# Performance work log

Hardware: AMD Instinct MI355X
Metric: run time of the kernel (lower is better)

## Reference

```python
import jax, jax.numpy as jnp
import numpy as np

D_K = 64  # key dim -> temperature = sqrt(64) = 8.0


def setup_inputs() -> dict:
    key = jax.random.key(0)
    k1, k2, k3, k4 = jax.random.split(key, 4)
    N, P, d_k, d_v = 4, 4096, 64, 256
    k_src = jax.random.normal(k1, (N, P, d_k), dtype=jnp.float32)
    v_src = jax.random.normal(k2, (N, P, d_v), dtype=jnp.float32)
    q_tgr = jax.random.normal(k3, (N, P, d_k), dtype=jnp.float32)
    # 1x1 conv (d_v -> d_v) == per-position linear; kaiming-style init
    W_fc = jax.random.normal(k4, (d_v, d_v), dtype=jnp.float32) * (1.0 / np.sqrt(d_v))
    b_fc = jnp.zeros((d_v,), dtype=jnp.float32)
    return {"k_src": k_src, "v_src": v_src, "q_tgr": q_tgr, "W_fc": W_fc, "b_fc": b_fc}


def reference(k_src, v_src, q_tgr, W_fc, b_fc):
    temperature = jnp.asarray(np.sqrt(D_K), dtype=q_tgr.dtype)
    # scaled dot-product attention: [N,P,P] scores (mask=None, dropout=eval/identity)
    attn = jnp.einsum("npd,nqd->npq", q_tgr, k_src) / temperature
    attn = jax.nn.softmax(attn, axis=2)
    out = jnp.einsum("npq,nqc->npc", attn, v_src)  # [N,P,d_v]
    # fc: 1x1 conv over (N*P, C, 1, 1) == linear over channel dim
    out = jnp.einsum("npc,oc->npo", out, W_fc) + b_fc
    return out
```

## Files before the change

kernel.cpp:

```cpp
#include <hip/hip_runtime.h>
#include <hip/hip_bf16.h>

#define NB 4
#define PSEQ 4096
#define DK 64
#define DV 256

typedef __attribute__((ext_vector_type(8))) short short8;
typedef __attribute__((ext_vector_type(16))) float f32x16;
typedef __attribute__((ext_vector_type(4))) unsigned int uint4v;

__device__ __forceinline__ float bf2f(unsigned short u) {
    union { unsigned int i; float f; } v; v.i = ((unsigned int)u) << 16; return v.f;
}
__device__ __forceinline__ unsigned short f2bf(float f) {
    union { float f; unsigned int i; } v; v.f = f;
    return (unsigned short)((v.i + 0x7fffu + ((v.i >> 16) & 1u)) >> 16);
}

__device__ __forceinline__ short8 gload16(const void* p) {
    short8 r;
    asm volatile("global_load_dwordx4 %0, %1, off"
                 : "=v"(r) : "v"(p) : "memory");
    return r;
}

__global__ __launch_bounds__(256) void prep_all(
    const float* __restrict__ q, const float* __restrict__ k,
    const float* __restrict__ wfc, const float* __restrict__ v,
    unsigned short* __restrict__ Qh, unsigned short* __restrict__ Ql,
    unsigned short* __restrict__ Kp,
    unsigned short* __restrict__ Wb, unsigned short* __restrict__ Vp) {
    __shared__ float tile[64][65];
    const int b = blockIdx.x, tid = threadIdx.x;
    if (b < 1024) {
        const int i = (b * 256 + tid) * 4;
        float4 x = *reinterpret_cast<const float4*>(q + i);
        ushort4 h, l;
        h.x = f2bf(x.x); l.x = f2bf(x.x - bf2f(h.x));
        h.y = f2bf(x.y); l.y = f2bf(x.y - bf2f(h.y));
        h.z = f2bf(x.z); l.z = f2bf(x.z - bf2f(h.z));
        h.w = f2bf(x.w); l.w = f2bf(x.w - bf2f(h.w));
        *reinterpret_cast<ushort4*>(Qh + i) = h;
        *reinterpret_cast<ushort4*>(Ql + i) = l;
    } else if (b < 1536) {
        const int idx = b - 1024;
        const int n = idx >> 7, g = idx & 127;
        const int d = tid >> 6, lane = tid & 63;
        const int l31 = lane & 31, hi = lane >> 5;
        const float* src = k + ((size_t)(n * PSEQ + g * 32 + l31)) * DK + d * 16 + hi * 8;
        float x[8];
        *reinterpret_cast<float4*>(&x[0]) = *reinterpret_cast<const float4*>(src);
        *reinterpret_cast<float4*>(&x[4]) = *reinterpret_cast<const float4*>(src + 4);
        short8 o;
#pragma unroll
        for (int j = 0; j < 8; ++j) o[j] = (short)f2bf(x[j]);
        *reinterpret_cast<short8*>(
            Kp + (((size_t)n * 512 + g * 4 + d) * 64 + lane) * 8) = o;
    } else if (b < 1600) {
        const int i = ((b - 1536) * 256 + tid) * 4;
        float4 x = *reinterpret_cast<const float4*>(wfc + i);
        ushort4 h;
        h.x = f2bf(x.x); h.y = f2bf(x.y); h.z = f2bf(x.z); h.w = f2bf(x.w);
        *reinterpret_cast<ushort4*>(Wb + i) = h;
    } else {
        const int vtid = b - 1600;
        const int k0 = (vtid & 63) * 64, c0 = ((vtid >> 6) & 3) * 64, n = vtid >> 8;
        const int gb = (vtid & 63) * 2;
        const int cb = ((vtid >> 6) & 3) * 2;
        const float* vn = v + (size_t)n * PSEQ * DV;
        const int tx = tid & 15, ty = tid >> 4;
#pragma unroll
        for (int rep = 0; rep < 4; ++rep) {
            int r = ty + rep * 16;
            float4 d = *reinterpret_cast<const float4*>(vn + (size_t)(k0 + r) * DV + c0 + tx * 4);
            tile[r][tx * 4 + 0] = d.x; tile[r][tx * 4 + 1] = d.y;
            tile[r][tx * 4 + 2] = d.z; tile[r][tx * 4 + 3] = d.w;
        }
        __syncthreads();
#pragma unroll
        for (int uu = 0; uu < 2; ++uu) {
            const int u = tid * 2 + uu;
            const int lane = u & 63;
            const int slot = (u >> 6) & 1;
            const int c32l = (u >> 7) & 1;
            const int gl   = (u >> 8) & 1;
            const int l31 = lane & 31, hi = lane >> 5;
            const int keyl = gl * 32 + slot * 16 + hi * 8;
            const int chl = c32l * 32 + l31;
            short8 o;
#pragma unroll
            for (int j = 0; j < 8; ++j) o[j] = (short)f2bf(tile[keyl + j][chl]);
            *reinterpret_cast<short8*>(
                Vp + ((((size_t)n * 128 + gb + gl) * 8 + cb + c32l) * 2 + slot) * 512
                   + lane * 8) = o;
        }
    }
}

__global__ __launch_bounds__(256, 2) void attn_wave(
    const unsigned short* __restrict__ Kp,
    const unsigned short* __restrict__ Qh,
    const unsigned short* __restrict__ Ql,
    const unsigned short* __restrict__ Vp,
    const unsigned short* __restrict__ Wg,
    const float* __restrict__ Bg,
    float* __restrict__ Og)
{
    __shared__ float Of32[32][256];
    __shared__ unsigned short Omrg[32][260];
    __shared__ float Lsh[32];

    const int tid = threadIdx.x;
    const int w = tid >> 6;
    const int lane = tid & 63;
    const int l31 = lane & 31;
    const int hi = lane >> 5;
    const int kh = w >> 1;
    const int ch = w & 1;

    const int id = blockIdx.x;
    const int n = (id & 7) >> 1;
    const int q0 = ((id >> 3) * 2 + (id & 1)) * 32;

    if (tid < 32) Lsh[tid] = 0.f;
    __syncthreads();

    const unsigned short* Kpn = Kp + (size_t)n * 512 * 512;
    const unsigned short* Vpn = Vp + (size_t)n * 128 * 8 * 2 * 512;

    short8 qhf[4], qlf[4];
#pragma unroll
    for (int d = 0; d < 4; ++d) {
        const size_t a = ((size_t)n * PSEQ + q0 + l31) * DK + d * 16 + hi * 8;
        qhf[d] = *reinterpret_cast<const short8*>(Qh + a);
        qlf[d] = *reinterpret_cast<const short8*>(Ql + a);
    }

    const f32x16 Z16 = {0.f,0.f,0.f,0.f, 0.f,0.f,0.f,0.f,
                        0.f,0.f,0.f,0.f, 0.f,0.f,0.f,0.f};
    f32x16 oacc[4];
#pragma unroll
    for (int ct = 0; ct < 4; ++ct) oacc[ct] = Z16;

    float lsum = 0.f;
    const float SC = 0.125f * 1.44269504088896340736f;

    auto issueK = [&](int kt, short8 (&kf)[4]) {
        const int g = kh * 64 + kt;
#pragma unroll
        for (int d = 0; d < 4; ++d)
            kf[d] = gload16(Kpn + ((size_t)(g * 4 + d) * 64 + lane) * 8);
    };

    auto TILE = [&](int kt, short8 (&kfC)[4], short8 (&kfN)[4]) {
        asm volatile("s_waitcnt vmcnt(0)" ::: "memory");
        __builtin_amdgcn_sched_barrier(0);

        const int g = kh * 64 + kt;

        short8 vv[8];
#pragma unroll
        for (int ct = 0; ct < 4; ++ct) {
            const size_t vb = (((size_t)g * 8 + ch * 4 + ct) * 2) * 512;
            vv[ct]     = gload16(Vpn + vb + lane * 8);
            vv[4 + ct] = gload16(Vpn + vb + 512 + lane * 8);
        }

        f32x16 s = Z16;
        __builtin_amdgcn_s_setprio(1);
#pragma unroll
        for (int d = 0; d < 4; ++d)
            s = __builtin_amdgcn_mfma_f32_32x32x16_bf16(kfC[d], qhf[d], s, 0, 0, 0);
#pragma unroll
        for (int d = 0; d < 4; ++d)
            s = __builtin_amdgcn_mfma_f32_32x32x16_bf16(kfC[d], qlf[d], s, 0, 0, 0);
        __builtin_amdgcn_s_setprio(0);

        issueK(kt < 63 ? kt + 1 : 63, kfN);

        unsigned int pk[8];
        float lacc = 0.f;
#pragma unroll
        for (int j = 0; j < 8; ++j) {
            float p0 = exp2f(s[2 * j] * SC);
            float p1 = exp2f(s[2 * j + 1] * SC);
            lacc += p0 + p1;
            asm("v_cvt_pk_bf16_f32 %0, %1, %2" : "=v"(pk[j]) : "v"(p0), "v"(p1));
        }
        lsum += lacc;
        asm volatile("v_permlane32_swap_b32 %0, %1" : "+v"(pk[0]), "+v"(pk[2]));
        asm volatile("v_permlane32_swap_b32 %0, %1" : "+v"(pk[1]), "+v"(pk[3]));
        asm volatile("v_permlane32_swap_b32 %0, %1" : "+v"(pk[4]), "+v"(pk[6]));
        asm volatile("v_permlane32_swap_b32 %0, %1" : "+v"(pk[5]), "+v"(pk[7]));
        union { uint4v u; short8 s8; } cvt0, cvt1;
        cvt0.u = (uint4v){pk[0], pk[1], pk[2], pk[3]};
        cvt1.u = (uint4v){pk[4], pk[5], pk[6], pk[7]};
        const short8 pa0 = cvt0.s8, pa1 = cvt1.s8;

        asm volatile("s_waitcnt vmcnt(4)" ::: "memory");
        __builtin_amdgcn_sched_barrier(0);

        __builtin_amdgcn_s_setprio(1);
#pragma unroll
        for (int ct = 0; ct < 4; ++ct)
            oacc[ct] = __builtin_amdgcn_mfma_f32_32x32x16_bf16(pa0, vv[ct], oacc[ct], 0, 0, 0);
#pragma unroll
        for (int ct = 0; ct < 4; ++ct)
            oacc[ct] = __builtin_amdgcn_mfma_f32_32x32x16_bf16(pa1, vv[4 + ct], oacc[ct], 0, 0, 0);
        __builtin_amdgcn_s_setprio(0);
    };

    short8 kfA[4], kfB[4];
    issueK(0, kfA);

#pragma unroll 1
    for (int kt = 0; kt < 64; kt += 2) {
        TILE(kt, kfA, kfB);
        TILE(kt + 1, kfB, kfA);
    }
    asm volatile("s_waitcnt vmcnt(0)" ::: "memory");

    lsum += __shfl_xor(lsum, 32, 64);
    if (ch == 0 && lane < 32) atomicAdd(&Lsh[l31], lsum);

    const int cb0 = ch * 128;
    if (kh == 0) {
#pragma unroll
        for (int ct = 0; ct < 4; ++ct)
#pragma unroll
            for (int r = 0; r < 16; ++r) {
                const int row = (r & 3) + 8 * (r >> 2) + 4 * hi;
                Of32[row][cb0 + ct * 32 + l31] = oacc[ct][r];
            }
    }
    __syncthreads();
    if (kh == 1) {
#pragma unroll
        for (int ct = 0; ct < 4; ++ct)
#pragma unroll
            for (int r = 0; r < 16; ++r) {
                const int row = (r & 3) + 8 * (r >> 2) + 4 * hi;
                Of32[row][cb0 + ct * 32 + l31] += oacc[ct][r];
            }
    }
    __syncthreads();

    {
        const int row = tid >> 3;
        const int col0 = (tid & 7) * 32;
        const float il = 1.0f / Lsh[row];
#pragma unroll
        for (int j = 0; j < 8; ++j) {
            float4 xv = *reinterpret_cast<const float4*>(&Of32[row][col0 + j * 4]);
            ushort4 o;
            o.x = f2bf(xv.x * il); o.y = f2bf(xv.y * il);
            o.z = f2bf(xv.z * il); o.w = f2bf(xv.w * il);
            *reinterpret_cast<ushort4*>(&Omrg[row][col0 + j * 4]) = o;
        }
    }
    __syncthreads();

    f32x16 fa0 = Z16, fa1 = Z16;
#pragma unroll
    for (int slot = 0; slot < 16; ++slot) {
        short8 af = *reinterpret_cast<const short8*>(&Omrg[l31][slot * 16 + hi * 8]);
        short8 w0 = *reinterpret_cast<const short8*>(
            Wg + (size_t)(w * 64 + l31) * DV + slot * 16 + hi * 8);
        short8 w1 = *reinterpret_cast<const short8*>(
            Wg + (size_t)(w * 64 + 32 + l31) * DV + slot * 16 + hi * 8);
        fa0 = __builtin_amdgcn_mfma_f32_32x32x16_bf16(af, w0, fa0, 0, 0, 0);
        fa1 = __builtin_amdgcn_mfma_f32_32x32x16_bf16(af, w1, fa1, 0, 0, 0);
    }
    {
        const float b0 = Bg[w * 64 + l31], b1 = Bg[w * 64 + 32 + l31];
#pragma unroll
        for (int r = 0; r < 16; ++r) {
            const int row = (r & 3) + 8 * (r >> 2) + 4 * hi;
            const size_t orow = ((size_t)n * PSEQ + q0 + row) * DV;
            Og[orow + w * 64 + l31]      = fa0[r] + b0;
            Og[orow + w * 64 + 32 + l31] = fa1[r] + b1;
        }
    }
}

extern "C" void kernel_launch(void* const* d_in, const int* in_sizes, int n_in,
                              void* d_out, int out_size, void* d_ws, size_t ws_size,
                              hipStream_t stream) {
    const float* k_src = (const float*)d_in[0];
    const float* v_src = (const float*)d_in[1];
    const float* q_tgr = (const float*)d_in[2];
    const float* W_fc  = (const float*)d_in[3];
    const float* b_fc  = (const float*)d_in[4];
    float* out = (float*)d_out;

    char* wsb = (char*)d_ws;
    unsigned short* Vp = (unsigned short*)(wsb);
    unsigned short* Qh = (unsigned short*)(wsb + 8388608);
    unsigned short* Ql = (unsigned short*)(wsb + 10485760);
    unsigned short* Kp = (unsigned short*)(wsb + 12582912);
    unsigned short* Wb = (unsigned short*)(wsb + 14680064);

    prep_all<<<2624, 256, 0, stream>>>(q_tgr, k_src, W_fc, v_src,
                                       Qh, Ql, Kp, Wb, Vp);
    attn_wave<<<512, 256, 0, stream>>>(Kp, Qh, Ql, Vp, Wb, b_fc, out);
}
```

Baseline: 180.0 us.

## Split attention blocks by value-channel half and combine FC output with atomics

Each block now owns one 32-row query tile and one half of the value channels. Its four waves split the key range into quarters instead of a 2x2 key/channel split, which doubles the grid to 1024 blocks. Partial FC products over the two channel halves are accumulated into the output with float atomics, so a memset of the output is added before the launch. The aim is more parallelism and occupancy, but the QK scores and softmax are now computed twice per query tile, and the change adds a four-step serialized LDS reduction plus atomic-add traffic.

```diff
diff --git a/kernel.cpp b/kernel.cpp
--- a/kernel.cpp
+++ b/kernel.cpp
@@ -107,8 +107,8 @@
     const float* __restrict__ Bg,
     float* __restrict__ Og)
 {
-    __shared__ float Of32[32][256];
-    __shared__ unsigned short Omrg[32][260];
+    __shared__ float Of32[32][128];
+    __shared__ unsigned short Omrg[32][132];
     __shared__ float Lsh[32];
 
     const int tid = threadIdx.x;
@@ -116,12 +116,11 @@
     const int lane = tid & 63;
     const int l31 = lane & 31;
     const int hi = lane >> 5;
-    const int kh = w >> 1;
-    const int ch = w & 1;
 
     const int id = blockIdx.x;
-    const int n = (id & 7) >> 1;
-    const int q0 = ((id >> 3) * 2 + (id & 1)) * 32;
+    const int n   = (id & 7) >> 1;
+    const int chb = id & 1;
+    const int q0  = (id >> 3) * 32;
 
     if (tid < 32) Lsh[tid] = 0.f;
     __syncthreads();
@@ -147,7 +146,7 @@
     const float SC = 0.125f * 1.44269504088896340736f;
 
     auto issueK = [&](int kt, short8 (&kf)[4]) {
-        const int g = kh * 64 + kt;
+        const int g = w * 32 + kt;
 #pragma unroll
         for (int d = 0; d < 4; ++d)
             kf[d] = gload16(Kpn + ((size_t)(g * 4 + d) * 64 + lane) * 8);
@@ -157,12 +156,12 @@
         asm volatile("s_waitcnt vmcnt(0)" ::: "memory");
         __builtin_amdgcn_sched_barrier(0);
 
-        const int g = kh * 64 + kt;
+        const int g = w * 32 + kt;
 
         short8 vv[8];
 #pragma unroll
         for (int ct = 0; ct < 4; ++ct) {
-            const size_t vb = (((size_t)g * 8 + ch * 4 + ct) * 2) * 512;
+            const size_t vb = (((size_t)g * 8 + chb * 4 + ct) * 2) * 512;
             vv[ct]     = gload16(Vpn + vb + lane * 8);
             vv[4 + ct] = gload16(Vpn + vb + 512 + lane * 8);
         }
@@ -177,7 +176,7 @@
             s = __builtin_amdgcn_mfma_f32_32x32x16_bf16(kfC[d], qlf[d], s, 0, 0, 0);
         __builtin_amdgcn_s_setprio(0);
 
-        issueK(kt < 63 ? kt + 1 : 63, kfN);
+        issueK(kt < 31 ? kt + 1 : 31, kfN);
 
         unsigned int pk[8];
         float lacc = 0.f;
@@ -215,43 +214,62 @@
     issueK(0, kfA);
 
 #pragma unroll 1
-    for (int kt = 0; kt < 64; kt += 2) {
+    for (int kt = 0; kt < 32; kt += 2) {
         TILE(kt, kfA, kfB);
         TILE(kt + 1, kfB, kfA);
     }
     asm volatile("s_waitcnt vmcnt(0)" ::: "memory");
 
     lsum += __shfl_xor(lsum, 32, 64);
-    if (ch == 0 && lane < 32) atomicAdd(&Lsh[l31], lsum);
-
-    const int cb0 = ch * 128;
-    if (kh == 0) {
+    if (lane < 32) atomicAdd(&Lsh[l31], lsum);
+
+    if (w == 0) {
 #pragma unroll
         for (int ct = 0; ct < 4; ++ct)
 #pragma unroll
             for (int r = 0; r < 16; ++r) {
                 const int row = (r & 3) + 8 * (r >> 2) + 4 * hi;
-                Of32[row][cb0 + ct * 32 + l31] = oacc[ct][r];
+                Of32[row][ct * 32 + l31] = oacc[ct][r];
             }
     }
     __syncthreads();
-    if (kh == 1) {
+    if (w == 1) {
 #pragma unroll
         for (int ct = 0; ct < 4; ++ct)
 #pragma unroll
             for (int r = 0; r < 16; ++r) {
                 const int row = (r & 3) + 8 * (r >> 2) + 4 * hi;
-                Of32[row][cb0 + ct * 32 + l31] += oacc[ct][r];
+                Of32[row][ct * 32 + l31] += oacc[ct][r];
+            }
+    }
+    __syncthreads();
+    if (w == 2) {
+#pragma unroll
+        for (int ct = 0; ct < 4; ++ct)
+#pragma unroll
+            for (int r = 0; r < 16; ++r) {
+                const int row = (r & 3) + 8 * (r >> 2) + 4 * hi;
+                Of32[row][ct * 32 + l31] += oacc[ct][r];
+            }
+    }
+    __syncthreads();
+    if (w == 3) {
+#pragma unroll
+        for (int ct = 0; ct < 4; ++ct)
+#pragma unroll
+            for (int r = 0; r < 16; ++r) {
+                const int row = (r & 3) + 8 * (r >> 2) + 4 * hi;
+                Of32[row][ct * 32 + l31] += oacc[ct][r];
             }
     }
     __syncthreads();
 
     {
         const int row = tid >> 3;
-        const int col0 = (tid & 7) * 32;
+        const int col0 = (tid & 7) * 16;
         const float il = 1.0f / Lsh[row];
 #pragma unroll
-        for (int j = 0; j < 8; ++j) {
+        for (int j = 0; j < 4; ++j) {
             float4 xv = *reinterpret_cast<const float4*>(&Of32[row][col0 + j * 4]);
             ushort4 o;
             o.x = f2bf(xv.x * il); o.y = f2bf(xv.y * il);
@@ -263,23 +281,24 @@
 
     f32x16 fa0 = Z16, fa1 = Z16;
 #pragma unroll
-    for (int slot = 0; slot < 16; ++slot) {
+    for (int slot = 0; slot < 8; ++slot) {
         short8 af = *reinterpret_cast<const short8*>(&Omrg[l31][slot * 16 + hi * 8]);
         short8 w0 = *reinterpret_cast<const short8*>(
-            Wg + (size_t)(w * 64 + l31) * DV + slot * 16 + hi * 8);
+            Wg + (size_t)(w * 64 + l31) * DV + chb * 128 + slot * 16 + hi * 8);
         short8 w1 = *reinterpret_cast<const short8*>(
-            Wg + (size_t)(w * 64 + 32 + l31) * DV + slot * 16 + hi * 8);
+            Wg + (size_t)(w * 64 + 32 + l31) * DV + chb * 128 + slot * 16 + hi * 8);
         fa0 = __builtin_amdgcn_mfma_f32_32x32x16_bf16(af, w0, fa0, 0, 0, 0);
         fa1 = __builtin_amdgcn_mfma_f32_32x32x16_bf16(af, w1, fa1, 0, 0, 0);
     }
     {
-        const float b0 = Bg[w * 64 + l31], b1 = Bg[w * 64 + 32 + l31];
+        const float b0 = chb == 0 ? Bg[w * 64 + l31] : 0.f;
+        const float b1 = chb == 0 ? Bg[w * 64 + 32 + l31] : 0.f;
 #pragma unroll
         for (int r = 0; r < 16; ++r) {
             const int row = (r & 3) + 8 * (r >> 2) + 4 * hi;
             const size_t orow = ((size_t)n * PSEQ + q0 + row) * DV;
-            Og[orow + w * 64 + l31]      = fa0[r] + b0;
-            Og[orow + w * 64 + 32 + l31] = fa1[r] + b1;
+            atomicAdd(&Og[orow + w * 64 + l31],      fa0[r] + b0);
+            atomicAdd(&Og[orow + w * 64 + 32 + l31], fa1[r] + b1);
         }
     }
 }
@@ -303,5 +322,6 @@
 
     prep_all<<<2624, 256, 0, stream>>>(q_tgr, k_src, W_fc, v_src,
                                        Qh, Ql, Kp, Wb, Vp);
-    attn_wave<<<512, 256, 0, stream>>>(Kp, Qh, Ql, Vp, Wb, b_fc, out);
-}
+    hipMemsetAsync(d_out, 0, (size_t)out_size, stream);
+    attn_wave<<<1024, 256, 0, stream>>>(Kp, Qh, Ql, Vp, Wb, b_fc, out);
+}
```

Result: slower. 187.6 us (+4.2%).
